# Performance work log

Measured on AMD Instinct MI355X. Metric: run time of the kernel, lower is better.

Reference implementation:

```python
import jax, jax.numpy as jnp
import numpy as np

N_NODES = 100_000
N_EDGES = 1_000_000
N_GRAPHS = 2048
F_IN, N_HEADS, HEAD_DIM = 128, 2, 32
NEG_SLOPE = 0.2


def seg_softmax(logits, seg, num):
    # numerically stable scatter-softmax over segments (leading axis)
    m = jax.ops.segment_max(logits, seg, num_segments=num)
    e = jnp.exp(logits - m[seg])
    s = jax.ops.segment_sum(e, seg, num_segments=num)
    return e / s[seg]


def setup_inputs() -> dict:
    key = jax.random.key(0)
    ks = jax.random.split(key, 10)
    HC = N_HEADS * HEAD_DIM
    x = jax.random.normal(ks[0], (N_NODES, F_IN), jnp.float32)
    edge_index = jax.random.randint(ks[1], (2, N_EDGES), 0, N_NODES, jnp.int32)
    batch = jnp.sort(jax.random.randint(ks[2], (N_NODES,), 0, N_GRAPHS, jnp.int32))
    sc_in = 1.0 / np.sqrt(F_IN)
    sc_hc = 1.0 / np.sqrt(HC)
    W_l = jax.random.normal(ks[3], (F_IN, HC), jnp.float32) * sc_in
    W_r = jax.random.normal(ks[4], (F_IN, HC), jnp.float32) * sc_in
    att = jax.random.normal(ks[5], (N_HEADS, HEAD_DIM), jnp.float32) * (1.0 / np.sqrt(HEAD_DIM))
    bias = jnp.zeros((HC,), jnp.float32)
    w_rel = jax.random.normal(ks[6], (HC,), jnp.float32) * sc_hc
    w_root = jax.random.normal(ks[7], (HC,), jnp.float32) * sc_hc
    b_score = jnp.zeros((1,), jnp.float32)
    return {"x": x, "edge_index": edge_index, "batch": batch, "W_l": W_l,
            "W_r": W_r, "att": att, "bias": bias, "w_rel": w_rel,
            "w_root": w_root, "b_score": b_score}


def reference(x, edge_index, batch, W_l, W_r, att, bias, w_rel, w_root, b_score):
    N = x.shape[0]
    H, C = att.shape
    src, dst = edge_index[0], edge_index[1]
    # --- GATv2Conv (add_self_loops=True, concat heads, negative_slope=0.2) ---
    loop = jnp.arange(N, dtype=src.dtype)
    s = jnp.concatenate([src, loop])  # source j
    d = jnp.concatenate([dst, loop])  # target i
    xl = (x @ W_l).reshape(N, H, C)   # lin_l -> source features
    xr = (x @ W_r).reshape(N, H, C)   # lin_r -> target features
    e = jax.nn.leaky_relu(xl[s] + xr[d], NEG_SLOPE)       # [E', H, C]
    logits = jnp.einsum('ehc,hc->eh', e, att)              # [E', H]
    alpha = seg_softmax(logits, d, N)                      # softmax over incoming edges per target
    h = jax.ops.segment_sum(xl[s] * alpha[:, :, None], d, num_segments=N)
    h = h.reshape(N, H * C) + bias                         # conv output (data.x)
    # --- SAGPooling(min_score=-1): softmax(GraphConv score) keeps all nodes ---
    aggr = jax.ops.segment_sum(h[src], dst, num_segments=N)  # GraphConv neighbor add-aggr
    score = aggr @ w_rel + h @ w_root + b_score              # [N]
    sm = seg_softmax(score, batch, N_GRAPHS)
    px = h * sm[:, None]
    # --- global_add_pool + global_mean_pool ---
    add = jax.ops.segment_sum(px, batch, num_segments=N_GRAPHS)
    cnt = jax.ops.segment_sum(jnp.ones((N,), px.dtype), batch, num_segments=N_GRAPHS)
    mean = add / jnp.maximum(cnt, 1.0)[:, None]
    return add + mean  # global_emb [N_GRAPHS, H*C]
```

## Files before the change

### kernel.cpp

```cpp
#include <hip/hip_runtime.h>
#include <hip/hip_bf16.h>

#define N_NODES 100000
#define N_EDGES 1000000
#define N_GRAPHS 2048
#define F_IN 128
#define NEG_SLOPE 0.2f
#define E_TOT (N_EDGES + N_NODES)
#define SCAN_BLK 98
#define GEMM_BLOCKS 782
#define HIST_BLOCKS ((E_TOT + 255) / 256)
#define NODE_BLOCKS ((N_NODES + 255) / 256)

typedef short  bf16x8 __attribute__((ext_vector_type(8)));
typedef float  f32x16 __attribute__((ext_vector_type(16)));

__device__ __forceinline__ short f2bf(float f) {
    unsigned u = __float_as_uint(f);
    unsigned r = (u + 0x7fffu + ((u >> 16) & 1u)) >> 16;
    return (short)r;
}
__device__ __forceinline__ float bf2f(short h) {
    return __uint_as_float(((unsigned)(unsigned short)h) << 16);
}

template <int CTRL>
__device__ __forceinline__ float dpp_add(float x) {
    return x + __int_as_float(__builtin_amdgcn_update_dpp(
        0, __float_as_int(x), CTRL, 0xf, 0xf, true));
}
__device__ __forceinline__ float head_sum_bcast(float x) {
    x = dpp_add<0x111>(x);
    x = dpp_add<0x112>(x);
    x = dpp_add<0x114>(x);
    x = dpp_add<0x118>(x);
    x = dpp_add<0x142>(x);
    return __int_as_float(__builtin_amdgcn_ds_swizzle(__float_as_int(x), 0x03E0));
}
__device__ __forceinline__ float full_sum64(float x) {
    x = dpp_add<0x111>(x);
    x = dpp_add<0x112>(x);
    x = dpp_add<0x114>(x);
    x = dpp_add<0x118>(x);
    x = dpp_add<0x142>(x);
    x = dpp_add<0x143>(x);
    return x;
}

__global__ __launch_bounds__(256) void k_gemm_hist(const float* __restrict__ x,
                                                   const float* __restrict__ Wl,
                                                   const float* __restrict__ Wr,
                                                   const int* __restrict__ ei,
                                                   float* __restrict__ xlr,
                                                   int* __restrict__ counts,
                                                   int* __restrict__ rank_) {
    if (blockIdx.x >= GEMM_BLOCKS) {
        int e = (blockIdx.x - GEMM_BLOCKS) * 256 + threadIdx.x;
        if (e < E_TOT) {
            int d = (e < N_EDGES) ? ei[N_EDGES + e] : (e - N_EDGES);
            rank_[e] = atomicAdd(&counts[d], 1);
        }
        return;
    }
    __shared__ short wt[2][128][136];
    int tid = threadIdx.x;
    {
        int k  = tid >> 1;
        int cq = tid & 1;
        const float* Wsrc = cq ? Wr : Wl;
#pragma unroll
        for (int u = 0; u < 16; ++u) {
            int c0 = u * 4;
            float4 wv = *(const float4*)(Wsrc + (size_t)k * 64 + c0);
            float vv[4] = {wv.x, wv.y, wv.z, wv.w};
#pragma unroll
            for (int q = 0; q < 4; ++q) {
                int c = cq * 64 + c0 + q;
                short hi = f2bf(vv[q]);
                wt[0][c][k] = hi;
                wt[1][c][k] = f2bf(vv[q] - bf2f(hi));
            }
        }
    }
    __syncthreads();
    int lane = tid & 63, w = tid >> 6;
    int m = lane & 31, half = lane >> 5;
    int row = blockIdx.x * 128 + w * 32 + m;
    bool rv = row < N_NODES;
    const float* xrow = x + (size_t)(rv ? row : 0) * F_IN;
    f32x16 acc[4];
#pragma unroll
    for (int t = 0; t < 4; ++t)
#pragma unroll
        for (int i = 0; i < 16; ++i) acc[t][i] = 0.f;

#pragma unroll
    for (int kt = 0; kt < 8; ++kt) {
        int kb = kt * 16 + half * 8;
        float4 xa = rv ? *(const float4*)(xrow + kb)
                       : make_float4(0.f, 0.f, 0.f, 0.f);
        float4 xb = rv ? *(const float4*)(xrow + kb + 4)
                       : make_float4(0.f, 0.f, 0.f, 0.f);
        float xs[8] = {xa.x, xa.y, xa.z, xa.w, xb.x, xb.y, xb.z, xb.w};
        bf16x8 ahi, alo;
#pragma unroll
        for (int j = 0; j < 8; ++j) {
            short hi = f2bf(xs[j]);
            ahi[j] = hi;
            alo[j] = f2bf(xs[j] - bf2f(hi));
        }
#pragma unroll
        for (int t = 0; t < 4; ++t) {
            int n = t * 32 + m;
            bf16x8 bhi = *(const bf16x8*)&wt[0][n][kb];
            bf16x8 blo = *(const bf16x8*)&wt[1][n][kb];
            acc[t] = __builtin_amdgcn_mfma_f32_32x32x16_bf16(ahi, bhi, acc[t], 0, 0, 0);
            acc[t] = __builtin_amdgcn_mfma_f32_32x32x16_bf16(ahi, blo, acc[t], 0, 0, 0);
            acc[t] = __builtin_amdgcn_mfma_f32_32x32x16_bf16(alo, bhi, acc[t], 0, 0, 0);
        }
    }
    int r0 = blockIdx.x * 128 + w * 32 + 4 * half;
#pragma unroll
    for (int t = 0; t < 4; ++t)
#pragma unroll
        for (int reg = 0; reg < 16; ++reg) {
            int rr = r0 + (reg & 3) + 8 * (reg >> 2);
            if (rr < N_NODES)
                xlr[(size_t)rr * 128 + t * 32 + m] = acc[t][reg];
        }
}

__global__ __launch_bounds__(256) void k_scanA(const int* __restrict__ counts,
                                               int* __restrict__ rowptr,
                                               int* __restrict__ bsum) {
    __shared__ int sh[256];
    int t = threadIdx.x, b = blockIdx.x;
    int base = b * 1024 + t * 4;
    int v[4]; int s = 0;
#pragma unroll
    for (int i = 0; i < 4; ++i) {
        int idx = base + i;
        v[i] = (idx < N_NODES) ? counts[idx] : 0;
        s += v[i];
    }
    sh[t] = s; __syncthreads();
    for (int off = 1; off < 256; off <<= 1) {
        int xv = (t >= off) ? sh[t - off] : 0;
        __syncthreads();
        sh[t] += xv;
        __syncthreads();
    }
    int run = sh[t] - s;
    if (t == 255) bsum[b] = sh[255];
#pragma unroll
    for (int i = 0; i < 4; ++i) {
        int idx = base + i;
        if (idx < N_NODES) rowptr[idx] = run;
        run += v[i];
    }
}

__global__ __launch_bounds__(256) void k_scanC_bounds(int* __restrict__ rowptr,
                                                      const int* __restrict__ bsum,
                                                      const int* __restrict__ batch,
                                                      int* __restrict__ start) {
    if (blockIdx.x < NODE_BLOCKS) {
        int i = blockIdx.x * 256 + threadIdx.x;
        int target = blockIdx.x >> 2;
        int lane = threadIdx.x & 63;
        int p = 0;
        if (lane < target)                    p  = bsum[lane];
        if (lane + 64 < target && lane + 64 < SCAN_BLK) p += bsum[lane + 64];
#pragma unroll
        for (int o = 1; o < 64; o <<= 1) p += __shfl_xor(p, o, 64);
        if (i < N_NODES) rowptr[i] += p;
        if (blockIdx.x == 0 && threadIdx.x == 0) rowptr[N_NODES] = E_TOT;
    } else {
        int i = (blockIdx.x - NODE_BLOCKS) * 256 + threadIdx.x;
        if (i >= N_NODES) return;
        int bi = batch[i];
        int bp = (i == 0) ? -1 : batch[i - 1];
        for (int g = bp + 1; g <= bi; ++g) start[g] = i;
        if (i == N_NODES - 1)
            for (int g = bi + 1; g <= N_GRAPHS; ++g) start[g] = N_NODES;
    }
}

__global__ __launch_bounds__(256) void k_scatter(const int* __restrict__ ei,
                                                 const int* __restrict__ rowptr,
                                                 const int* __restrict__ rank_,
                                                 int* __restrict__ sorted_src) {
    int e = blockIdx.x * 256 + threadIdx.x;
    if (e >= E_TOT) return;
    int s, d;
    if (e < N_EDGES) { s = ei[e]; d = ei[N_EDGES + e]; }
    else             { s = d = e - N_EDGES; }
    sorted_src[rowptr[d] + rank_[e]] = s;
}

__global__ __launch_bounds__(256) void k_gat(const float* __restrict__ xlr,
                                             const int* __restrict__ rowptr,
                                             const int* __restrict__ sorted_src,
                                             const float* __restrict__ att,
                                             const float* __restrict__ bias,
                                             const float* __restrict__ w_rel,
                                             const float* __restrict__ w_root,
                                             float* __restrict__ hfeat,
                                             float* __restrict__ tbuf,
                                             float* __restrict__ rbuf) {
    int lane = threadIdx.x & 63;
    int du = __builtin_amdgcn_readfirstlane(blockIdx.x * 4 + (threadIdx.x >> 6));
    if (du >= N_NODES) return;
    float xr_l  = xlr[(size_t)du * 128 + 64 + lane];
    float att_l = att[lane];
    int j0 = __builtin_amdgcn_readfirstlane(rowptr[du]);
    int j1 = __builtin_amdgcn_readfirstlane(rowptr[du + 1]);
    float m = -1e30f, wsum = 0.f, acc = 0.f;
    for (int jc = j0; jc < j1; jc += 8) {
        int n = j1 - jc;
        int jj = jc + (lane & 7);
        if (jj > j1 - 1) jj = j1 - 1;
        int sv = sorted_src[jj];
        float p[8], xv[8];
#pragma unroll
        for (int i = 0; i < 8; ++i) {
            int s = __builtin_amdgcn_readlane(sv, i);
            const float* ps = xlr + (size_t)(unsigned)s * 128;
            xv[i] = ps[lane];
        }
#pragma unroll
        for (int i = 0; i < 8; ++i) {
            float v = xv[i] + xr_l;
            v = (v > 0.f) ? v : NEG_SLOPE * v;
            p[i] = v * att_l;
        }
#pragma unroll
        for (int i = 0; i < 8; ++i)
            p[i] = head_sum_bcast(p[i]);
#pragma unroll
        for (int i = 0; i < 8; ++i)
            if (i >= n) p[i] = -1e30f;
        float mc = p[0];
#pragma unroll
        for (int i = 1; i < 8; ++i) mc = fmaxf(mc, p[i]);
        float cws = 0.f, cacc = 0.f;
#pragma unroll
        for (int i = 0; i < 8; ++i) {
            float wgt = __expf(p[i] - mc);
            cws += wgt;
            cacc += wgt * xv[i];
        }
        float mnew = fmaxf(m, mc);
        float fo = __expf(m - mnew), fn = __expf(mc - mnew);
        wsum = wsum * fo + cws * fn;
        acc  = acc  * fo + cacc * fn;
        m = mnew;
    }
    float h = acc / wsum + bias[lane];
    hfeat[(size_t)du * 64 + lane] = h;
    float a = full_sum64(h * w_rel[lane]);
    float b = full_sum64(h * w_root[lane]);
    if (lane == 63) { tbuf[du] = a; rbuf[du] = b; }
}

__global__ __launch_bounds__(256) void k_pool(const int* __restrict__ rowptr,
                                              const int* __restrict__ sorted_src,
                                              const float* __restrict__ t,
                                              const float* __restrict__ r,
                                              const float* __restrict__ b_score,
                                              float* __restrict__ score,
                                              const float* __restrict__ h,
                                              const int* __restrict__ start,
                                              float* __restrict__ out) {
    __shared__ float sh[4];
    __shared__ float shacc[4][64];
    int g = blockIdx.x;
    int tid = threadIdx.x, w = tid >> 6, lane = tid & 63;
    int n0 = start[g], n1 = start[g + 1];
    int cnt = n1 - n0;
    if (cnt <= 0) { if (tid < 64) out[(size_t)g * 64 + tid] = 0.f; return; }
    float bsc = b_score[0];
    for (int i = n0 + tid; i < n1; i += 256) {
        int jj0 = rowptr[i], jj1 = rowptr[i + 1];
        float sum = 0.f;
        int j = jj0;
        for (; j + 4 <= jj1; j += 4) {
            int s0 = sorted_src[j], s1 = sorted_src[j + 1];
            int s2 = sorted_src[j + 2], s3 = sorted_src[j + 3];
            sum += t[s0] + t[s1] + t[s2] + t[s3];
        }
        for (; j < jj1; ++j) sum += t[sorted_src[j]];
        score[i] = sum - t[i] + r[i] + bsc;
    }
    __syncthreads();
    float m = -1e30f;
    for (int i = n0 + tid; i < n1; i += 256) m = fmaxf(m, score[i]);
#pragma unroll
    for (int o = 32; o; o >>= 1) m = fmaxf(m, __shfl_xor(m, o, 64));
    if (lane == 0) sh[w] = m;
    __syncthreads();
    m = fmaxf(fmaxf(sh[0], sh[1]), fmaxf(sh[2], sh[3]));
    float ssum = 0.f;
    for (int i = n0 + tid; i < n1; i += 256) ssum += __expf(score[i] - m);
#pragma unroll
    for (int o = 32; o; o >>= 1) ssum += __shfl_xor(ssum, o, 64);
    __syncthreads();
    if (lane == 0) sh[w] = ssum;
    __syncthreads();
    ssum = sh[0] + sh[1] + sh[2] + sh[3];
    float acc = 0.f;
    for (int i = n0 + w; i < n1; i += 4)
        acc += __expf(score[i] - m) * h[(size_t)i * 64 + lane];
    shacc[w][lane] = acc;
    __syncthreads();
    if (w == 0) {
        float tot = shacc[0][lane] + shacc[1][lane] + shacc[2][lane] + shacc[3][lane];
        out[(size_t)g * 64 + lane] = tot * (1.f + 1.f / (float)cnt) / ssum;
    }
}

extern "C" void kernel_launch(void* const* d_in, const int* in_sizes, int n_in,
                              void* d_out, int out_size, void* d_ws, size_t ws_size,
                              hipStream_t stream) {
    const float* x      = (const float*)d_in[0];
    const int*   ei     = (const int*)d_in[1];
    const int*   batch  = (const int*)d_in[2];
    const float* Wl     = (const float*)d_in[3];
    const float* Wr     = (const float*)d_in[4];
    const float* att    = (const float*)d_in[5];
    const float* bias   = (const float*)d_in[6];
    const float* w_rel  = (const float*)d_in[7];
    const float* w_root = (const float*)d_in[8];
    const float* b_sc   = (const float*)d_in[9];

    char* ws = (char*)d_ws;
    size_t off = 0;
    auto alloc = [&](size_t bytes) { void* p = ws + off; off += (bytes + 255) & ~255ull; return p; };
    float* xlr        = (float*)alloc((size_t)N_NODES * 128 * 4);
    float* hfeat      = (float*)alloc((size_t)N_NODES * 64 * 4);
    int*   sorted_src = (int*)  alloc((size_t)E_TOT * 4);
    int*   rank_      = (int*)  alloc((size_t)E_TOT * 4);
    int*   counts     = (int*)  alloc((size_t)N_NODES * 4);
    int*   rowptr     = (int*)  alloc((size_t)(N_NODES + 1) * 4);
    int*   bsum       = (int*)  alloc((size_t)SCAN_BLK * 4);
    float* tbuf       = (float*)alloc((size_t)N_NODES * 4);
    float* rbuf       = (float*)alloc((size_t)N_NODES * 4);
    float* score      = (float*)alloc((size_t)N_NODES * 4);
    int*   start      = (int*)  alloc((size_t)(N_GRAPHS + 1) * 4);

    (void)hipMemsetAsync(counts, 0, (size_t)N_NODES * 4, stream);

    k_gemm_hist   <<<GEMM_BLOCKS + HIST_BLOCKS, 256, 0, stream>>>(x, Wl, Wr, ei, xlr, counts, rank_);
    k_scanA       <<<SCAN_BLK, 256, 0, stream>>>(counts, rowptr, bsum);
    k_scanC_bounds<<<NODE_BLOCKS * 2, 256, 0, stream>>>(rowptr, bsum, batch, start);
    k_scatter     <<<(E_TOT + 255) / 256, 256, 0, stream>>>(ei, rowptr, rank_, sorted_src);
    k_gat         <<<(N_NODES + 3) / 4, 256, 0, stream>>>(xlr, rowptr, sorted_src, att, bias,
                                                          w_rel, w_root, hfeat, tbuf, rbuf);
    k_pool        <<<N_GRAPHS, 256, 0, stream>>>(rowptr, sorted_src, tbuf, rbuf, b_sc,
                                                 score, hfeat, start, (float*)d_out);
}
```

Baseline: 249.0 us.

## Drop online-max softmax in GAT edge loop and split pooling gathers across lane quads

The GAT aggregation no longer tracks a running max for the edge softmax. It exponentiates the logits directly and processes full 8-edge chunks without masking, then handles the tail in masked chunks of 4. This removes the max reductions and rescale exponentials, but risks overflow if a logit grows large. In the pooling kernel, each node's neighbor score sum is now spread over 4 lanes and reduced with DPP, which improves load parallelism for nodes with uneven degree.

Result: no change. 253.3 us (+1.7%).

```diff
diff --git a/kernel.cpp b/kernel.cpp
--- a/kernel.cpp
+++ b/kernel.cpp
@@ -44,6 +44,11 @@
     x = dpp_add<0x118>(x);
     x = dpp_add<0x142>(x);
     x = dpp_add<0x143>(x);
+    return x;
+}
+__device__ __forceinline__ float quad_sum(float x) {
+    x = dpp_add<0xB1>(x);
+    x = dpp_add<0x4E>(x);
     return x;
 }
 
@@ -215,18 +220,15 @@
     float att_l = att[lane];
     int j0 = __builtin_amdgcn_readfirstlane(rowptr[du]);
     int j1 = __builtin_amdgcn_readfirstlane(rowptr[du + 1]);
-    float m = -1e30f, wsum = 0.f, acc = 0.f;
-    for (int jc = j0; jc < j1; jc += 8) {
-        int n = j1 - jc;
-        int jj = jc + (lane & 7);
-        if (jj > j1 - 1) jj = j1 - 1;
-        int sv = sorted_src[jj];
+    float wsum = 0.f, acc = 0.f;
+    int jc = j0;
+    for (; jc + 8 <= j1; jc += 8) {
+        int sv = sorted_src[jc + (lane & 7)];
         float p[8], xv[8];
 #pragma unroll
         for (int i = 0; i < 8; ++i) {
             int s = __builtin_amdgcn_readlane(sv, i);
-            const float* ps = xlr + (size_t)(unsigned)s * 128;
-            xv[i] = ps[lane];
+            xv[i] = (xlr + (size_t)(unsigned)s * 128)[lane];
         }
 #pragma unroll
         for (int i = 0; i < 8; ++i) {
@@ -238,23 +240,38 @@
         for (int i = 0; i < 8; ++i)
             p[i] = head_sum_bcast(p[i]);
 #pragma unroll
-        for (int i = 0; i < 8; ++i)
-            if (i >= n) p[i] = -1e30f;
-        float mc = p[0];
-#pragma unroll
-        for (int i = 1; i < 8; ++i) mc = fmaxf(mc, p[i]);
-        float cws = 0.f, cacc = 0.f;
-#pragma unroll
         for (int i = 0; i < 8; ++i) {
-            float wgt = __expf(p[i] - mc);
-            cws += wgt;
-            cacc += wgt * xv[i];
-        }
-        float mnew = fmaxf(m, mc);
-        float fo = __expf(m - mnew), fn = __expf(mc - mnew);
-        wsum = wsum * fo + cws * fn;
-        acc  = acc  * fo + cacc * fn;
-        m = mnew;
+            float w = __expf(p[i]);
+            wsum += w;
+            acc += w * xv[i];
+        }
+    }
+    for (; jc < j1; jc += 4) {
+        int n = j1 - jc;
+        int jj = jc + (lane & 3);
+        if (jj > j1 - 1) jj = j1 - 1;
+        int sv = sorted_src[jj];
+        float p[4], xv[4];
+#pragma unroll
+        for (int i = 0; i < 4; ++i) {
+            int s = __builtin_amdgcn_readlane(sv, i);
+            xv[i] = (xlr + (size_t)(unsigned)s * 128)[lane];
+        }
+#pragma unroll
+        for (int i = 0; i < 4; ++i) {
+            float v = xv[i] + xr_l;
+            v = (v > 0.f) ? v : NEG_SLOPE * v;
+            p[i] = v * att_l;
+        }
+#pragma unroll
+        for (int i = 0; i < 4; ++i)
+            p[i] = head_sum_bcast(p[i]);
+#pragma unroll
+        for (int i = 0; i < 4; ++i) {
+            float w = (i < n) ? __expf(p[i]) : 0.f;
+            wsum += w;
+            acc += w * xv[i];
+        }
     }
     float h = acc / wsum + bias[lane];
     hfeat[(size_t)du * 64 + lane] = h;
@@ -280,17 +297,16 @@
     int cnt = n1 - n0;
     if (cnt <= 0) { if (tid < 64) out[(size_t)g * 64 + tid] = 0.f; return; }
     float bsc = b_score[0];
-    for (int i = n0 + tid; i < n1; i += 256) {
-        int jj0 = rowptr[i], jj1 = rowptr[i + 1];
+    for (int base = n0; base < n1; base += 64) {
+        int i = base + (tid >> 2);
         float sum = 0.f;
-        int j = jj0;
-        for (; j + 4 <= jj1; j += 4) {
-            int s0 = sorted_src[j], s1 = sorted_src[j + 1];
-            int s2 = sorted_src[j + 2], s3 = sorted_src[j + 3];
-            sum += t[s0] + t[s1] + t[s2] + t[s3];
-        }
-        for (; j < jj1; ++j) sum += t[sorted_src[j]];
-        score[i] = sum - t[i] + r[i] + bsc;
+        int jj0 = 0, jj1 = 0;
+        if (i < n1) { jj0 = rowptr[i]; jj1 = rowptr[i + 1]; }
+        for (int j = jj0 + (tid & 3); j < jj1; j += 4)
+            sum += t[sorted_src[j]];
+        sum = quad_sum(sum);
+        if (i < n1 && (tid & 3) == 0)
+            score[i] = sum - t[i] + r[i] + bsc;
     }
     __syncthreads();
     float m = -1e30f;
```
